# Kernel optimization log

Measured on AMD Instinct MI355X. Metric: run time of the kernel, lower is better.

Reference implementation:

```python
import jax, jax.numpy as jnp
import numpy as np

N_HEADS = 2
WINDOW = 4
BLOCK = 256


def _get_rel_emb(emb, length):
    # emb: [1, 2*WINDOW+1, K] -> [1, 2*length-1, K]
    pad = max(length - (WINDOW + 1), 0)
    start = max((WINDOW + 1) - length, 0)
    e = jnp.pad(emb, ((0, 0), (pad, pad), (0, 0)))
    return e[:, start:start + 2 * length - 1]


def _rel_to_abs(x):
    # x: [b, h, l, 2l-1] -> [b, h, l, l] (skew trick)
    b, h, l, _ = x.shape
    x = jnp.pad(x, ((0, 0), (0, 0), (0, 0), (0, 1))).reshape(b, h, 2 * l * l)
    x = jnp.pad(x, ((0, 0), (0, 0), (0, l - 1))).reshape(b, h, l + 1, 2 * l - 1)
    return x[:, :, :l, l - 1:]


def _abs_to_rel(x):
    # x: [b, h, l, l] -> [b, h, l, 2l-1] (inverse skew)
    b, h, l, _ = x.shape
    x = jnp.pad(x, ((0, 0), (0, 0), (0, 0), (0, l - 1))).reshape(b, h, l * (2 * l - 1))
    x = jnp.pad(x, ((0, 0), (0, 0), (l, 0))).reshape(b, h, l, 2 * l)
    return x[:, :, :, 1:]


def _attention(x, c, attn_mask, Wq, bq, Wk, bk, Wv, bv, Wo, bo, emb_rel_k, emb_rel_v):
    B, C, T = x.shape
    H, K = N_HEADS, C // N_HEADS
    # projections (torch Linear on [B,T,C])
    q = (jnp.einsum('bct,cd->btd', x, Wq) + bq).reshape(B, T, H, K).transpose(0, 2, 1, 3)
    k = (jnp.einsum('bct,cd->btd', c, Wk) + bk).reshape(B, T, H, K).transpose(0, 2, 1, 3)
    v = (jnp.einsum('bct,cd->btd', c, Wv) + bv).reshape(B, T, H, K).transpose(0, 2, 1, 3)
    qs = q / jnp.sqrt(jnp.float32(K))
    scores = jnp.einsum('bhtk,bhsk->bhts', qs, k)  # [B,H,T,T]
    # relative-position key logits (heads_share=True -> single table)
    rel_k = _get_rel_emb(emb_rel_k, T)[0]          # [2T-1, K]
    rel_logits = jnp.einsum('bhtk,rk->bhtr', qs, rel_k)
    scores = scores + _rel_to_abs(rel_logits)
    # proximal bias: -log1p(|i-j|)
    r = jnp.arange(T, dtype=jnp.float32)
    scores = scores - jnp.log1p(jnp.abs(r[:, None] - r[None, :]))[None, None]
    # attn mask + block-local mask (block mask active because mask is given)
    ij = jnp.arange(T)
    block_ok = jnp.abs(ij[:, None] - ij[None, :]) <= BLOCK
    valid = (attn_mask != 0) & block_ok[None, None]
    scores = jnp.where(valid, scores, jnp.float32(-1e4))
    p = jax.nn.softmax(scores, axis=-1)
    out = jnp.einsum('bhts,bhsk->bhtk', p, v)
    # relative-position value contribution
    rel_v = _get_rel_emb(emb_rel_v, T)[0]          # [2T-1, K]
    out = out + jnp.einsum('bhtr,rk->bhtk', _abs_to_rel(p), rel_v)
    out = out.transpose(0, 2, 1, 3).reshape(B, T, C)
    y = jnp.einsum('btd,do->bto', out, Wo) + bo
    return y.transpose(0, 2, 1)  # [B, out_channels, T]


def setup_inputs() -> dict:
    key = jax.random.key(0)
    ks = jax.random.split(key, 8)
    B, C, T = 4, 192, 2048
    K = C // N_HEADS
    s = jnp.float32(0.05)
    rel_std = jnp.float32(K ** -0.5)
    return {
        'x': jax.random.normal(ks[0], (B, C, T), jnp.float32),
        'c': jax.random.normal(ks[1], (B, C, T), jnp.float32),
        'Wq': jax.random.normal(ks[2], (C, C), jnp.float32) * s,
        'bq': jnp.zeros((C,), jnp.float32),
        'Wk': jax.random.normal(ks[3], (C, C), jnp.float32) * s,
        'bk': jnp.zeros((C,), jnp.float32),
        'Wv': jax.random.normal(ks[4], (C, C), jnp.float32) * s,
        'bv': jnp.zeros((C,), jnp.float32),
        'Wo': jax.random.normal(ks[5], (C, C), jnp.float32) * s,
        'bo': jnp.zeros((C,), jnp.float32),
        'emb_rel_k': jax.random.normal(ks[6], (1, 2 * WINDOW + 1, K), jnp.float32) * rel_std,
        'emb_rel_v': jax.random.normal(ks[7], (1, 2 * WINDOW + 1, K), jnp.float32) * rel_std,
        'attn_mask': jnp.ones((B, 1, T, T), jnp.int32),
    }


def reference(x, c, Wq, bq, Wk, bk, Wv, bv, Wo, bo, emb_rel_k, emb_rel_v, attn_mask):
    return _attention(x, c, attn_mask, Wq, bq, Wk, bk, Wv, bv, Wo, bo, emb_rel_k, emb_rel_v)
```

## Files before the change

### kernel.cpp

```cpp
#include <hip/hip_runtime.h>
#include <hip/hip_bf16.h>

#define B_DIM 4
#define C_DIM 192
#define T_SEQ 2048
#define H_DIM 2
#define K_DIM 96
#define BAND 256
#define IT 16
#define WSLOT 544
#define W_P 548
#define PMW 17

typedef __attribute__((ext_vector_type(8))) short bf16x8;
typedef __attribute__((ext_vector_type(4))) short bf16x4;
typedef __attribute__((ext_vector_type(4))) float f32x4;
#define MFMA16 __builtin_amdgcn_mfma_f32_16x16x32_bf16

__device__ __forceinline__ float bfbits2f(short s) {
    union { short s; __hip_bfloat16 h; } u; u.s = s; return __bfloat162float(u.h);
}
__device__ __forceinline__ short f2bf_bits(float f) {
    union { __hip_bfloat16 h; short s; } u; u.h = __float2bfloat16(f); return u.s;
}

#define OFF_WT(m)  ((size_t)(m)*73728)
#define OFF_BQS    ((size_t)294912)
#define OFF_RELKBF ((size_t)295680)
#define OFF_PM     ((size_t)298752)
#define OFF_QBF    ((size_t)855808)
#define OFF_KBF    (OFF_QBF + 3145728)
#define OFF_VTB    (OFF_KBF + 3145728)
#define OFF_OBTC   (OFF_VTB + 3145728)

__global__ __launch_bounds__(256)
void prep_kernel(const float* __restrict__ Wq, const float* __restrict__ Wk,
                 const float* __restrict__ Wv, const float* __restrict__ Wo,
                 const float* __restrict__ bq, const float* __restrict__ relk,
                 const int* __restrict__ mask, char* __restrict__ ws)
{
    const float qscale = 0.10206207261596577f;
    const int bidx = blockIdx.x;
    const int tid  = threadIdx.x;

    if (bidx < 576) {
        const size_t idx = (size_t)bidx*256 + tid;
        const int mi  = (int)(idx / 36864);
        const int rem = (int)(idx % 36864);
        const int c = rem / C_DIM, d = rem % C_DIM;
        const float* src = (mi == 0) ? Wq : (mi == 1) ? Wk : (mi == 2) ? Wv : Wo;
        float v = src[c*C_DIM + d];
        if (mi == 0) v *= qscale;
        ((short*)(ws + OFF_WT(mi)))[d*C_DIM + c] = f2bf_bits(v);
        return;
    }
    if (bidx < 1120) {
        const int idx = (bidx - 576)*256 + tid;
        const int b = idx / (T_SEQ*PMW);
        const int rem = idx % (T_SEQ*PMW);
        const int i = rem / PMW, w = rem % PMW;
        const int jlo = max(0, (i & ~15) - BAND);
        const int* mrow = mask + ((size_t)b*T_SEQ + i)*T_SEQ;
        unsigned bits = 0;
        #pragma unroll
        for (int g4 = 0; g4 < 8; ++g4) {
            const int jg = jlo + 32*w + 4*g4;
            if (jg + 3 < T_SEQ) {
                const int4 mv = *reinterpret_cast<const int4*>(mrow + jg);
                bits |= (unsigned)(mv.x != 0) << (4*g4);
                bits |= (unsigned)(mv.y != 0) << (4*g4+1);
                bits |= (unsigned)(mv.z != 0) << (4*g4+2);
                bits |= (unsigned)(mv.w != 0) << (4*g4+3);
            } else {
                #pragma unroll
                for (int e = 0; e < 4; ++e)
                    if (jg + e < T_SEQ && mrow[jg+e] != 0) bits |= 1u << (4*g4+e);
            }
        }
        ((unsigned*)(ws + OFF_PM))[idx] = bits;
        return;
    }
    if (tid < C_DIM)
        ((float*)(ws + OFF_BQS))[tid] = bq[tid]*qscale;
    short* rkb = (short*)(ws + OFF_RELKBF);
    for (int idx = tid; idx < 16*K_DIM; idx += 256) {
        const int row = idx / K_DIM;
        rkb[idx] = (row < 9) ? f2bf_bits(relk[idx]) : (short)0;
    }
}

__global__ __launch_bounds__(256)
void proj_kernel(const float* __restrict__ x, const float* __restrict__ cin,
                 const float* __restrict__ bk, const float* __restrict__ bv,
                 char* __restrict__ ws)
{
    __shared__ short xs[IT*C_DIM];
    __shared__ short cs[IT*C_DIM];
    const int b   = blockIdx.x >> 7;
    const int t0  = (blockIdx.x & 127) * IT;
    const int tid = threadIdx.x;
    const int wave = tid >> 6, lane = tid & 63;
    const int q4 = lane >> 4, lr = lane & 15;

    for (int l = tid; l < 768; l += 256) {
        const int cr = l >> 2, u = l & 3;
        const size_t off = (size_t)(b*C_DIM + cr)*T_SEQ + t0 + 4*u;
        const float4 xv = *reinterpret_cast<const float4*>(x + off);
        const float4 cv = *reinterpret_cast<const float4*>(cin + off);
        xs[(4*u+0)*C_DIM + cr] = f2bf_bits(xv.x);
        xs[(4*u+1)*C_DIM + cr] = f2bf_bits(xv.y);
        xs[(4*u+2)*C_DIM + cr] = f2bf_bits(xv.z);
        xs[(4*u+3)*C_DIM + cr] = f2bf_bits(xv.w);
        cs[(4*u+0)*C_DIM + cr] = f2bf_bits(cv.x);
        cs[(4*u+1)*C_DIM + cr] = f2bf_bits(cv.y);
        cs[(4*u+2)*C_DIM + cr] = f2bf_bits(cv.z);
        cs[(4*u+3)*C_DIM + cr] = f2bf_bits(cv.w);
    }
    __syncthreads();

    const short* WqT = (const short*)(ws + OFF_WT(0));
    const short* WkT = (const short*)(ws + OFF_WT(1));
    const short* WvT = (const short*)(ws + OFF_WT(2));

    f32x4 qa[3], ka[3], va[3];
    #pragma unroll
    for (int j = 0; j < 3; ++j) {
        qa[j] = (f32x4){0,0,0,0}; ka[j] = (f32x4){0,0,0,0}; va[j] = (f32x4){0,0,0,0};
    }
    for (int kc = 0; kc < 6; ++kc) {
        const int ko = kc*32 + q4*8;
        const bf16x8 xf = *reinterpret_cast<const bf16x8*>(xs + lr*C_DIM + ko);
        const bf16x8 cf = *reinterpret_cast<const bf16x8*>(cs + lr*C_DIM + ko);
        #pragma unroll
        for (int j = 0; j < 3; ++j) {
            const int dt = 3*wave + j;
            const bf16x8 wqf = *reinterpret_cast<const bf16x8*>(WqT + (dt*16 + lr)*C_DIM + ko);
            const bf16x8 wkf = *reinterpret_cast<const bf16x8*>(WkT + (dt*16 + lr)*C_DIM + ko);
            const bf16x8 wvf = *reinterpret_cast<const bf16x8*>(WvT + (dt*16 + lr)*C_DIM + ko);
            qa[j] = MFMA16(xf, wqf, qa[j], 0, 0, 0);
            ka[j] = MFMA16(cf, wkf, ka[j], 0, 0, 0);
            va[j] = MFMA16(wvf, cf, va[j], 0, 0, 0);
        }
    }

    const float* bqs = (const float*)(ws + OFF_BQS);
    short* qbf = (short*)(ws + OFF_QBF);
    short* kbf = (short*)(ws + OFF_KBF);
    short* vtb = (short*)(ws + OFF_VTB);
    #pragma unroll
    for (int j = 0; j < 3; ++j) {
        const int dt = 3*wave + j;
        {
            const int d = dt*16 + lr, h = d/K_DIM, kk = d%K_DIM;
            const int bh = b*H_DIM + h;
            const float bq_v = bqs[d], bk_v = bk[d];
            #pragma unroll
            for (int e = 0; e < 4; ++e) {
                const int t = t0 + q4*4 + e;
                const size_t off = ((size_t)bh*T_SEQ + t)*K_DIM + kk;
                qbf[off] = f2bf_bits(qa[j][e] + bq_v);
                kbf[off] = f2bf_bits(ka[j][e] + bk_v);
            }
        }
        {
            #pragma unroll
            for (int e = 0; e < 4; ++e) {
                const int d = dt*16 + q4*4 + e, h = d/K_DIM, kk = d%K_DIM;
                const int bh = b*H_DIM + h;
                vtb[((size_t)bh*K_DIM + kk)*T_SEQ + t0 + lr] = f2bf_bits(va[j][e] + bv[d]);
            }
        }
    }
}

__global__ __launch_bounds__(256)
void attn_kernel(const float* __restrict__ relv, char* __restrict__ ws)
{
    __shared__ float p_s[IT*W_P];
    __shared__ float shbuf[864];

    const short* qbf = (const short*)(ws + OFF_QBF);
    const short* kbf = (const short*)(ws + OFF_KBF);
    const short* vtb = (const short*)(ws + OFF_VTB);
    const short* rkb = (const short*)(ws + OFF_RELKBF);
    const unsigned* pm = (const unsigned*)(ws + OFF_PM);
    short* obtc = (short*)(ws + OFF_OBTC);

    const int bh  = blockIdx.x >> 7;
    const int i0  = (blockIdx.x & 127) * IT;
    const int b   = bh / H_DIM;
    const int h   = bh % H_DIM;
    const int tid = threadIdx.x;
    const int wave = tid >> 6, lane = tid & 63;
    const int q4 = lane >> 4, lr = lane & 15;

    const int jlo  = max(0, i0 - BAND);
    const int jhi  = min(T_SEQ - 1, i0 + IT - 1 + BAND);
    const int wlen = jhi - jlo + 1;
    const size_t qkv_base = (size_t)bh * T_SEQ * K_DIM;

    float* lt = shbuf;
    float* rl = shbuf + 260;
    for (int idx = tid; idx < 257; idx += 256) lt[idx] = log1pf((float)idx);

    bf16x8 qa[3];
    {
        const short* qrow = qbf + qkv_base + (size_t)(i0 + lr)*K_DIM + q4*8;
        #pragma unroll
        for (int kc = 0; kc < 3; ++kc)
            qa[kc] = *reinterpret_cast<const bf16x8*>(qrow + kc*32);
    }

    for (int jt = wave; jt < WSLOT/16; jt += 4) {
        int jr = jlo + jt*16 + lr;
        if (jr > T_SEQ-1) jr = T_SEQ-1;
        const short* krow = kbf + qkv_base + (size_t)jr*K_DIM + q4*8;
        f32x4 s = {0.f,0.f,0.f,0.f};
        #pragma unroll
        for (int kc = 0; kc < 3; ++kc)
            s = MFMA16(qa[kc], *reinterpret_cast<const bf16x8*>(krow + kc*32), s, 0, 0, 0);
        #pragma unroll
        for (int e = 0; e < 4; ++e)
            p_s[(q4*4 + e)*W_P + jt*16 + lr] = s[e];
    }
    if (wave == 3) {
        const short* krow = rkb + lr*K_DIM + q4*8;
        f32x4 s = {0.f,0.f,0.f,0.f};
        #pragma unroll
        for (int kc = 0; kc < 3; ++kc)
            s = MFMA16(qa[kc], *reinterpret_cast<const bf16x8*>(krow + kc*32), s, 0, 0, 0);
        if (lr < 9) {
            #pragma unroll
            for (int e = 0; e < 4; ++e)
                rl[(q4*4 + e)*9 + lr] = s[e];
        }
    }
    __syncthreads();

    {
        const int r = tid >> 4, sj = tid & 15;
        const int i = i0 + r;
        const int pmrow = (b*T_SEQ + i)*PMW;
        float vals[36];
        float m = -INFINITY;
        #pragma unroll
        for (int mm = 0; mm < 9; ++mm) {
            const int j0 = 4*sj + 64*mm;
            float4 pv = make_float4(0.f,0.f,0.f,0.f);
            unsigned mb = 0;
            if (j0 < WSLOT) {
                pv = *reinterpret_cast<const float4*>(p_s + r*W_P + j0);
                mb = pm[pmrow + (j0 >> 5)] >> (j0 & 31);
            }
            const float pe[4] = {pv.x, pv.y, pv.z, pv.w};
            #pragma unroll
            for (int e = 0; e < 4; ++e) {
                const int j = j0 + e;
                float val = -INFINITY;
                if (j0 < WSLOT && j < wlen) {
                    const int jg = jlo + j, dd = jg - i;
                    const int ad = dd < 0 ? -dd : dd;
                    if (ad <= BAND && ((mb >> e) & 1)) {
                        val = pe[e] - lt[ad];
                        if ((unsigned)(dd + 4) <= 8u) val += rl[r*9 + dd + 4];
                    }
                }
                vals[mm*4 + e] = val;
                m = fmaxf(m, val);
            }
        }
        #pragma unroll
        for (int off = 8; off > 0; off >>= 1) m = fmaxf(m, __shfl_xor(m, off, 64));
        if (m == -INFINITY) m = 0.f;
        float ssum = 0.f;
        #pragma unroll
        for (int u = 0; u < 36; ++u) { vals[u] = __expf(vals[u] - m); ssum += vals[u]; }
        #pragma unroll
        for (int off = 8; off > 0; off >>= 1) ssum += __shfl_xor(ssum, off, 64);
        const float inv = ssum > 0.f ? 1.f/ssum : 0.f;
        short* pb = (short*)p_s;
        #pragma unroll
        for (int mm = 0; mm < 9; ++mm) {
            const int j0 = 4*sj + 64*mm;
            if (j0 < WSLOT) {
                bf16x4 w;
                #pragma unroll
                for (int e = 0; e < 4; ++e) w[e] = f2bf_bits(vals[mm*4+e]*inv);
                *reinterpret_cast<bf16x4*>(pb + r*(2*W_P) + j0) = w;
            }
        }
    }
    __syncthreads();

    for (int idx = tid; idx < 9*K_DIM; idx += 256) shbuf[idx] = relv[idx];

    const short* pb = (const short*)p_s;
    f32x4 o0 = {0.f,0.f,0.f,0.f}, o1 = {0.f,0.f,0.f,0.f};
    for (int kc = 0; kc < WSLOT/32; ++kc) {
        const bf16x8 pa = *reinterpret_cast<const bf16x8*>(pb + lr*(2*W_P) + kc*32 + q4*8);
        int tc = jlo + kc*32 + q4*8;
        if (tc > T_SEQ-8) tc = T_SEQ-8;
        const bf16x8 vb0 = *reinterpret_cast<const bf16x8*>(
            vtb + qkv_base + (size_t)(wave*16 + lr)*T_SEQ + tc);
        o0 = MFMA16(pa, vb0, o0, 0, 0, 0);
        if (wave < 2) {
            const bf16x8 vb1 = *reinterpret_cast<const bf16x8*>(
                vtb + qkv_base + (size_t)((wave+4)*16 + lr)*T_SEQ + tc);
            o1 = MFMA16(pa, vb1, o1, 0, 0, 0);
        }
    }
    __syncthreads();

    #pragma unroll
    for (int u = 0; u < 2; ++u) {
        if (u == 1 && wave >= 2) break;
        const int nt = (u == 0) ? wave : wave + 4;
        const f32x4 oc = (u == 0) ? o0 : o1;
        const int col = nt*16 + lr;
        #pragma unroll
        for (int e = 0; e < 4; ++e) {
            const int row = q4*4 + e;
            const int i = i0 + row;
            float v = oc[e];
            #pragma unroll
            for (int dd = 0; dd < 9; ++dd) {
                const int jg = i + dd - 4;
                if (jg >= 0 && jg < T_SEQ)
                    v += bfbits2f(pb[row*(2*W_P) + (jg - jlo)]) * shbuf[dd*K_DIM + col];
            }
            obtc[((size_t)b*T_SEQ + i)*C_DIM + h*K_DIM + col] = f2bf_bits(v);
        }
    }
}

__global__ __launch_bounds__(256)
void oproj_kernel(const float* __restrict__ bo, float* __restrict__ y,
                  const char* __restrict__ ws)
{
    const int b   = blockIdx.x >> 7;
    const int t0  = (blockIdx.x & 127) * 16;
    const int tid = threadIdx.x;
    const int wave = tid >> 6, lane = tid & 63;
    const int q4 = lane >> 4, lr = lane & 15;

    const short* WoT  = (const short*)(ws + OFF_WT(3));
    const short* obtc = (const short*)(ws + OFF_OBTC);

    f32x4 a[3];
    #pragma unroll
    for (int j = 0; j < 3; ++j) a[j] = (f32x4){0.f,0.f,0.f,0.f};
    for (int kc = 0; kc < 6; ++kc) {
        const int ko = kc*32 + q4*8;
        const bf16x8 bf = *reinterpret_cast<const bf16x8*>(
            obtc + ((size_t)b*T_SEQ + t0 + lr)*C_DIM + ko);
        #pragma unroll
        for (int j = 0; j < 3; ++j) {
            const bf16x8 af = *reinterpret_cast<const bf16x8*>(
                WoT + ((3*wave + j)*16 + lr)*C_DIM + ko);
            a[j] = MFMA16(af, bf, a[j], 0, 0, 0);
        }
    }
    #pragma unroll
    for (int j = 0; j < 3; ++j) {
        #pragma unroll
        for (int e = 0; e < 4; ++e) {
            const int d = (3*wave + j)*16 + q4*4 + e;
            y[((size_t)b*C_DIM + d)*T_SEQ + t0 + lr] = a[j][e] + bo[d];
        }
    }
}

extern "C" void kernel_launch(void* const* d_in, const int* in_sizes, int n_in,
                              void* d_out, int out_size, void* d_ws, size_t ws_size,
                              hipStream_t stream)
{
    const float* x    = (const float*)d_in[0];
    const float* c    = (const float*)d_in[1];
    const float* Wq   = (const float*)d_in[2];
    const float* bq   = (const float*)d_in[3];
    const float* Wk   = (const float*)d_in[4];
    const float* bk   = (const float*)d_in[5];
    const float* Wv   = (const float*)d_in[6];
    const float* bv   = (const float*)d_in[7];
    const float* Wo   = (const float*)d_in[8];
    const float* bo   = (const float*)d_in[9];
    const float* relk = (const float*)d_in[10];
    const float* relv = (const float*)d_in[11];
    const int*   mask = (const int*)d_in[12];
    float*       y    = (float*)d_out;
    char*        ws   = (char*)d_ws;

    hipLaunchKernelGGL(prep_kernel, dim3(1121), dim3(256), 0, stream,
                       Wq, Wk, Wv, Wo, bq, relk, mask, ws);
    hipLaunchKernelGGL(proj_kernel, dim3(B_DIM*(T_SEQ/16)), dim3(256), 0, stream,
                       x, c, bk, bv, ws);
    hipLaunchKernelGGL(attn_kernel, dim3(B_DIM*H_DIM*(T_SEQ/IT)), dim3(256), 0, stream,
                       relv, ws);
    hipLaunchKernelGGL(oproj_kernel, dim3(B_DIM*(T_SEQ/16)), dim3(256), 0, stream,
                       bo, y, ws);
}
```

Before: 179.8 us.

## Fuse output projection into attention kernel looping over heads per block

The attention kernel now handles both heads for a 16-row tile in sequence, keeps the per-head outputs in shared memory, and applies the output projection directly, so the separate oproj kernel and its bf16 intermediate buffer in global memory go away. The mask bits and log1p table are staged into shared memory once per block, and the log1p table is precomputed in prep. Weight transposition in prep is vectorised to float4 loads. In exchange the attention grid is halved to 512 blocks, which lowers parallelism and raises shared memory use per block.

```diff
diff --git a/kernel.cpp b/kernel.cpp
--- a/kernel.cpp
+++ b/kernel.cpp
@@ -27,11 +27,14 @@
 #define OFF_WT(m)  ((size_t)(m)*73728)
 #define OFF_BQS    ((size_t)294912)
 #define OFF_RELKBF ((size_t)295680)
-#define OFF_PM     ((size_t)298752)
-#define OFF_QBF    ((size_t)855808)
+#define OFF_LT     ((size_t)298752)
+#define OFF_PM     ((size_t)299840)
+#define OFF_QBF    ((size_t)856896)
 #define OFF_KBF    (OFF_QBF + 3145728)
 #define OFF_VTB    (OFF_KBF + 3145728)
-#define OFF_OBTC   (OFF_VTB + 3145728)
+
+#define SH_RL   260
+#define SH_RELV 408
 
 __global__ __launch_bounds__(256)
 void prep_kernel(const float* __restrict__ Wq, const float* __restrict__ Wk,
@@ -43,19 +46,23 @@
     const int bidx = blockIdx.x;
     const int tid  = threadIdx.x;
 
-    if (bidx < 576) {
-        const size_t idx = (size_t)bidx*256 + tid;
-        const int mi  = (int)(idx / 36864);
-        const int rem = (int)(idx % 36864);
+    if (bidx < 144) {
+        const size_t idx4 = ((size_t)bidx*256 + tid)*4;
+        const int mi  = (int)(idx4 / 36864);
+        const int rem = (int)(idx4 % 36864);
         const int c = rem / C_DIM, d = rem % C_DIM;
         const float* src = (mi == 0) ? Wq : (mi == 1) ? Wk : (mi == 2) ? Wv : Wo;
-        float v = src[c*C_DIM + d];
-        if (mi == 0) v *= qscale;
-        ((short*)(ws + OFF_WT(mi)))[d*C_DIM + c] = f2bf_bits(v);
+        float4 v = *reinterpret_cast<const float4*>(src + c*C_DIM + d);
+        if (mi == 0) { v.x *= qscale; v.y *= qscale; v.z *= qscale; v.w *= qscale; }
+        short* wt = (short*)(ws + OFF_WT(mi));
+        wt[(d+0)*C_DIM + c] = f2bf_bits(v.x);
+        wt[(d+1)*C_DIM + c] = f2bf_bits(v.y);
+        wt[(d+2)*C_DIM + c] = f2bf_bits(v.z);
+        wt[(d+3)*C_DIM + c] = f2bf_bits(v.w);
         return;
     }
-    if (bidx < 1120) {
-        const int idx = (bidx - 576)*256 + tid;
+    if (bidx < 688) {
+        const int idx = (bidx - 144)*256 + tid;
         const int b = idx / (T_SEQ*PMW);
         const int rem = idx % (T_SEQ*PMW);
         const int i = rem / PMW, w = rem % PMW;
@@ -87,6 +94,8 @@
         const int row = idx / K_DIM;
         rkb[idx] = (row < 9) ? f2bf_bits(relk[idx]) : (short)0;
     }
+    float* ltws = (float*)(ws + OFF_LT);
+    for (int idx = tid; idx < 257; idx += 256) ltws[idx] = log1pf((float)idx);
 }
 
 __global__ __launch_bounds__(256)
@@ -174,22 +183,23 @@
 }
 
 __global__ __launch_bounds__(256)
-void attn_kernel(const float* __restrict__ relv, char* __restrict__ ws)
+void attn_kernel(const float* __restrict__ relv, const float* __restrict__ bo,
+                 float* __restrict__ y, char* __restrict__ ws)
 {
     __shared__ float p_s[IT*W_P];
-    __shared__ float shbuf[864];
+    __shared__ float shbuf[1272];
+    __shared__ unsigned pml[IT*PMW];
+    __shared__ __align__(16) short ob[IT*C_DIM];
 
     const short* qbf = (const short*)(ws + OFF_QBF);
     const short* kbf = (const short*)(ws + OFF_KBF);
     const short* vtb = (const short*)(ws + OFF_VTB);
     const short* rkb = (const short*)(ws + OFF_RELKBF);
+    const float* ltws = (const float*)(ws + OFF_LT);
     const unsigned* pm = (const unsigned*)(ws + OFF_PM);
-    short* obtc = (short*)(ws + OFF_OBTC);
-
-    const int bh  = blockIdx.x >> 7;
+
+    const int b   = blockIdx.x >> 7;
     const int i0  = (blockIdx.x & 127) * IT;
-    const int b   = bh / H_DIM;
-    const int h   = bh % H_DIM;
     const int tid = threadIdx.x;
     const int wave = tid >> 6, lane = tid & 63;
     const int q4 = lane >> 4, lr = lane & 15;
@@ -197,175 +207,161 @@
     const int jlo  = max(0, i0 - BAND);
     const int jhi  = min(T_SEQ - 1, i0 + IT - 1 + BAND);
     const int wlen = jhi - jlo + 1;
-    const size_t qkv_base = (size_t)bh * T_SEQ * K_DIM;
 
     float* lt = shbuf;
-    float* rl = shbuf + 260;
-    for (int idx = tid; idx < 257; idx += 256) lt[idx] = log1pf((float)idx);
-
-    bf16x8 qa[3];
-    {
-        const short* qrow = qbf + qkv_base + (size_t)(i0 + lr)*K_DIM + q4*8;
-        #pragma unroll
-        for (int kc = 0; kc < 3; ++kc)
-            qa[kc] = *reinterpret_cast<const bf16x8*>(qrow + kc*32);
-    }
-
-    for (int jt = wave; jt < WSLOT/16; jt += 4) {
-        int jr = jlo + jt*16 + lr;
-        if (jr > T_SEQ-1) jr = T_SEQ-1;
-        const short* krow = kbf + qkv_base + (size_t)jr*K_DIM + q4*8;
-        f32x4 s = {0.f,0.f,0.f,0.f};
-        #pragma unroll
-        for (int kc = 0; kc < 3; ++kc)
-            s = MFMA16(qa[kc], *reinterpret_cast<const bf16x8*>(krow + kc*32), s, 0, 0, 0);
-        #pragma unroll
-        for (int e = 0; e < 4; ++e)
-            p_s[(q4*4 + e)*W_P + jt*16 + lr] = s[e];
-    }
-    if (wave == 3) {
-        const short* krow = rkb + lr*K_DIM + q4*8;
-        f32x4 s = {0.f,0.f,0.f,0.f};
-        #pragma unroll
-        for (int kc = 0; kc < 3; ++kc)
-            s = MFMA16(qa[kc], *reinterpret_cast<const bf16x8*>(krow + kc*32), s, 0, 0, 0);
-        if (lr < 9) {
+    float* rl = shbuf + SH_RL;
+    float* rv = shbuf + SH_RELV;
+    for (int idx = tid; idx < 257; idx += 256) lt[idx] = ltws[idx];
+    for (int idx = tid; idx < IT*PMW; idx += 256)
+        pml[idx] = pm[(b*T_SEQ + i0)*PMW + idx];
+    for (int idx = tid; idx < 9*K_DIM; idx += 256) rv[idx] = relv[idx];
+
+    for (int h = 0; h < H_DIM; ++h) {
+        const size_t qkv_base = (size_t)(b*H_DIM + h) * T_SEQ * K_DIM;
+
+        bf16x8 qa[3];
+        {
+            const short* qrow = qbf + qkv_base + (size_t)(i0 + lr)*K_DIM + q4*8;
+            #pragma unroll
+            for (int kc = 0; kc < 3; ++kc)
+                qa[kc] = *reinterpret_cast<const bf16x8*>(qrow + kc*32);
+        }
+
+        for (int jt = wave; jt < WSLOT/16; jt += 4) {
+            int jr = jlo + jt*16 + lr;
+            if (jr > T_SEQ-1) jr = T_SEQ-1;
+            const short* krow = kbf + qkv_base + (size_t)jr*K_DIM + q4*8;
+            f32x4 s = {0.f,0.f,0.f,0.f};
+            #pragma unroll
+            for (int kc = 0; kc < 3; ++kc)
+                s = MFMA16(qa[kc], *reinterpret_cast<const bf16x8*>(krow + kc*32), s, 0, 0, 0);
             #pragma unroll
             for (int e = 0; e < 4; ++e)
-                rl[(q4*4 + e)*9 + lr] = s[e];
-        }
-    }
-    __syncthreads();
-
-    {
-        const int r = tid >> 4, sj = tid & 15;
-        const int i = i0 + r;
-        const int pmrow = (b*T_SEQ + i)*PMW;
-        float vals[36];
-        float m = -INFINITY;
-        #pragma unroll
-        for (int mm = 0; mm < 9; ++mm) {
-            const int j0 = 4*sj + 64*mm;
-            float4 pv = make_float4(0.f,0.f,0.f,0.f);
-            unsigned mb = 0;
-            if (j0 < WSLOT) {
-                pv = *reinterpret_cast<const float4*>(p_s + r*W_P + j0);
-                mb = pm[pmrow + (j0 >> 5)] >> (j0 & 31);
-            }
-            const float pe[4] = {pv.x, pv.y, pv.z, pv.w};
+                p_s[(q4*4 + e)*W_P + jt*16 + lr] = s[e];
+        }
+        if (wave == 3) {
+            const short* krow = rkb + lr*K_DIM + q4*8;
+            f32x4 s = {0.f,0.f,0.f,0.f};
+            #pragma unroll
+            for (int kc = 0; kc < 3; ++kc)
+                s = MFMA16(qa[kc], *reinterpret_cast<const bf16x8*>(krow + kc*32), s, 0, 0, 0);
+            if (lr < 9) {
+                #pragma unroll
+                for (int e = 0; e < 4; ++e)
+                    rl[(q4*4 + e)*9 + lr] = s[e];
+            }
+        }
+        __syncthreads();
+
+        {
+            const int r = tid >> 4, sj = tid & 15;
+            const int i = i0 + r;
+            float vals[36];
+            float m = -INFINITY;
+            #pragma unroll
+            for (int mm = 0; mm < 9; ++mm) {
+                const int j0 = 4*sj + 64*mm;
+                float4 pv = make_float4(0.f,0.f,0.f,0.f);
+                unsigned mb = 0;
+                if (j0 < WSLOT) {
+                    pv = *reinterpret_cast<const float4*>(p_s + r*W_P + j0);
+                    mb = pml[r*PMW + (j0 >> 5)] >> (j0 & 31);
+                }
+                const float pe[4] = {pv.x, pv.y, pv.z, pv.w};
+                #pragma unroll
+                for (int e = 0; e < 4; ++e) {
+                    const int j = j0 + e;
+                    float val = -INFINITY;
+                    if (j0 < WSLOT && j < wlen) {
+                        const int jg = jlo + j, dd = jg - i;
+                        const int ad = dd < 0 ? -dd : dd;
+                        if (ad <= BAND && ((mb >> e) & 1)) {
+                            val = pe[e] - lt[ad];
+                            if ((unsigned)(dd + 4) <= 8u) val += rl[r*9 + dd + 4];
+                        }
+                    }
+                    vals[mm*4 + e] = val;
+                    m = fmaxf(m, val);
+                }
+            }
+            #pragma unroll
+            for (int off = 8; off > 0; off >>= 1) m = fmaxf(m, __shfl_xor(m, off, 64));
+            if (m == -INFINITY) m = 0.f;
+            float ssum = 0.f;
+            #pragma unroll
+            for (int u = 0; u < 36; ++u) { vals[u] = __expf(vals[u] - m); ssum += vals[u]; }
+            #pragma unroll
+            for (int off = 8; off > 0; off >>= 1) ssum += __shfl_xor(ssum, off, 64);
+            const float inv = ssum > 0.f ? 1.f/ssum : 0.f;
+            short* pb = (short*)p_s;
+            #pragma unroll
+            for (int mm = 0; mm < 9; ++mm) {
+                const int j0 = 4*sj + 64*mm;
+                if (j0 < WSLOT) {
+                    bf16x4 w;
+                    #pragma unroll
+                    for (int e = 0; e < 4; ++e) w[e] = f2bf_bits(vals[mm*4+e]*inv);
+                    *reinterpret_cast<bf16x4*>(pb + r*(2*W_P) + j0) = w;
+                }
+            }
+        }
+        __syncthreads();
+
+        const short* pb = (const short*)p_s;
+        f32x4 o0 = {0.f,0.f,0.f,0.f}, o1 = {0.f,0.f,0.f,0.f};
+        for (int kc = 0; kc < WSLOT/32; ++kc) {
+            const bf16x8 pa = *reinterpret_cast<const bf16x8*>(pb + lr*(2*W_P) + kc*32 + q4*8);
+            int tc = jlo + kc*32 + q4*8;
+            if (tc > T_SEQ-8) tc = T_SEQ-8;
+            const bf16x8 vb0 = *reinterpret_cast<const bf16x8*>(
+                vtb + qkv_base + (size_t)(wave*16 + lr)*T_SEQ + tc);
+            o0 = MFMA16(pa, vb0, o0, 0, 0, 0);
+            if (wave < 2) {
+                const bf16x8 vb1 = *reinterpret_cast<const bf16x8*>(
+                    vtb + qkv_base + (size_t)((wave+4)*16 + lr)*T_SEQ + tc);
+                o1 = MFMA16(pa, vb1, o1, 0, 0, 0);
+            }
+        }
+
+        #pragma unroll
+        for (int u = 0; u < 2; ++u) {
+            if (u == 1 && wave >= 2) break;
+            const int nt = (u == 0) ? wave : wave + 4;
+            const f32x4 oc = (u == 0) ? o0 : o1;
+            const int col = nt*16 + lr;
             #pragma unroll
             for (int e = 0; e < 4; ++e) {
-                const int j = j0 + e;
-                float val = -INFINITY;
-                if (j0 < WSLOT && j < wlen) {
-                    const int jg = jlo + j, dd = jg - i;
-                    const int ad = dd < 0 ? -dd : dd;
-                    if (ad <= BAND && ((mb >> e) & 1)) {
-                        val = pe[e] - lt[ad];
-                        if ((unsigned)(dd + 4) <= 8u) val += rl[r*9 + dd + 4];
-                    }
+                const int row = q4*4 + e;
+                const int i = i0 + row;
+                float v = oc[e];
+                #pragma unroll
+                for (int dd = 0; dd < 9; ++dd) {
+                    const int jg = i + dd - 4;
+                    if (jg >= 0 && jg < T_SEQ)
+                        v += bfbits2f(pb[row*(2*W_P) + (jg - jlo)]) * rv[dd*K_DIM + col];
                 }
-                vals[mm*4 + e] = val;
-                m = fmaxf(m, val);
-            }
-        }
-        #pragma unroll
-        for (int off = 8; off > 0; off >>= 1) m = fmaxf(m, __shfl_xor(m, off, 64));
-        if (m == -INFINITY) m = 0.f;
-        float ssum = 0.f;
-        #pragma unroll
-        for (int u = 0; u < 36; ++u) { vals[u] = __expf(vals[u] - m); ssum += vals[u]; }
-        #pragma unroll
-        for (int off = 8; off > 0; off >>= 1) ssum += __shfl_xor(ssum, off, 64);
-        const float inv = ssum > 0.f ? 1.f/ssum : 0.f;
-        short* pb = (short*)p_s;
-        #pragma unroll
-        for (int mm = 0; mm < 9; ++mm) {
-            const int j0 = 4*sj + 64*mm;
-            if (j0 < WSLOT) {
-                bf16x4 w;
-                #pragma unroll
-                for (int e = 0; e < 4; ++e) w[e] = f2bf_bits(vals[mm*4+e]*inv);
-                *reinterpret_cast<bf16x4*>(pb + r*(2*W_P) + j0) = w;
-            }
-        }
-    }
-    __syncthreads();
-
-    for (int idx = tid; idx < 9*K_DIM; idx += 256) shbuf[idx] = relv[idx];
-
-    const short* pb = (const short*)p_s;
-    f32x4 o0 = {0.f,0.f,0.f,0.f}, o1 = {0.f,0.f,0.f,0.f};
-    for (int kc = 0; kc < WSLOT/32; ++kc) {
-        const bf16x8 pa = *reinterpret_cast<const bf16x8*>(pb + lr*(2*W_P) + kc*32 + q4*8);
-        int tc = jlo + kc*32 + q4*8;
-        if (tc > T_SEQ-8) tc = T_SEQ-8;
-        const bf16x8 vb0 = *reinterpret_cast<const bf16x8*>(
-            vtb + qkv_base + (size_t)(wave*16 + lr)*T_SEQ + tc);
-        o0 = MFMA16(pa, vb0, o0, 0, 0, 0);
-        if (wave < 2) {
-            const bf16x8 vb1 = *reinterpret_cast<const bf16x8*>(
-                vtb + qkv_base + (size_t)((wave+4)*16 + lr)*T_SEQ + tc);
-            o1 = MFMA16(pa, vb1, o1, 0, 0, 0);
-        }
-    }
-    __syncthreads();
-
-    #pragma unroll
-    for (int u = 0; u < 2; ++u) {
-        if (u == 1 && wave >= 2) break;
-        const int nt = (u == 0) ? wave : wave + 4;
-        const f32x4 oc = (u == 0) ? o0 : o1;
-        const int col = nt*16 + lr;
-        #pragma unroll
-        for (int e = 0; e < 4; ++e) {
-            const int row = q4*4 + e;
-            const int i = i0 + row;
-            float v = oc[e];
-            #pragma unroll
-            for (int dd = 0; dd < 9; ++dd) {
-                const int jg = i + dd - 4;
-                if (jg >= 0 && jg < T_SEQ)
-                    v += bfbits2f(pb[row*(2*W_P) + (jg - jlo)]) * shbuf[dd*K_DIM + col];
-            }
-            obtc[((size_t)b*T_SEQ + i)*C_DIM + h*K_DIM + col] = f2bf_bits(v);
-        }
-    }
-}
-
-__global__ __launch_bounds__(256)
-void oproj_kernel(const float* __restrict__ bo, float* __restrict__ y,
-                  const char* __restrict__ ws)
-{
-    const int b   = blockIdx.x >> 7;
-    const int t0  = (blockIdx.x & 127) * 16;
-    const int tid = threadIdx.x;
-    const int wave = tid >> 6, lane = tid & 63;
-    const int q4 = lane >> 4, lr = lane & 15;
-
-    const short* WoT  = (const short*)(ws + OFF_WT(3));
-    const short* obtc = (const short*)(ws + OFF_OBTC);
-
-    f32x4 a[3];
-    #pragma unroll
-    for (int j = 0; j < 3; ++j) a[j] = (f32x4){0.f,0.f,0.f,0.f};
-    for (int kc = 0; kc < 6; ++kc) {
-        const int ko = kc*32 + q4*8;
-        const bf16x8 bf = *reinterpret_cast<const bf16x8*>(
-            obtc + ((size_t)b*T_SEQ + t0 + lr)*C_DIM + ko);
-        #pragma unroll
-        for (int j = 0; j < 3; ++j) {
-            const bf16x8 af = *reinterpret_cast<const bf16x8*>(
-                WoT + ((3*wave + j)*16 + lr)*C_DIM + ko);
-            a[j] = MFMA16(af, bf, a[j], 0, 0, 0);
-        }
-    }
+                ob[row*C_DIM + h*K_DIM + col] = f2bf_bits(v);
+            }
+        }
+        __syncthreads();
+    }
+
+    const short* WoT = (const short*)(ws + OFF_WT(3));
     #pragma unroll
     for (int j = 0; j < 3; ++j) {
+        const int dt = 3*wave + j;
+        f32x4 a = {0.f,0.f,0.f,0.f};
+        #pragma unroll
+        for (int kc = 0; kc < 6; ++kc) {
+            const int ko = kc*32 + q4*8;
+            const bf16x8 bf = *reinterpret_cast<const bf16x8*>(ob + lr*C_DIM + ko);
+            const bf16x8 af = *reinterpret_cast<const bf16x8*>(WoT + (dt*16 + lr)*C_DIM + ko);
+            a = MFMA16(af, bf, a, 0, 0, 0);
+        }
         #pragma unroll
         for (int e = 0; e < 4; ++e) {
-            const int d = (3*wave + j)*16 + q4*4 + e;
-            y[((size_t)b*C_DIM + d)*T_SEQ + t0 + lr] = a[j][e] + bo[d];
+            const int d = dt*16 + q4*4 + e;
+            y[((size_t)b*C_DIM + d)*T_SEQ + i0 + lr] = a[e] + bo[d];
         }
     }
 }
@@ -390,12 +386,10 @@
     float*       y    = (float*)d_out;
     char*        ws   = (char*)d_ws;
 
-    hipLaunchKernelGGL(prep_kernel, dim3(1121), dim3(256), 0, stream,
+    hipLaunchKernelGGL(prep_kernel, dim3(689), dim3(256), 0, stream,
                        Wq, Wk, Wv, Wo, bq, relk, mask, ws);
     hipLaunchKernelGGL(proj_kernel, dim3(B_DIM*(T_SEQ/16)), dim3(256), 0, stream,
                        x, c, bk, bv, ws);
-    hipLaunchKernelGGL(attn_kernel, dim3(B_DIM*H_DIM*(T_SEQ/IT)), dim3(256), 0, stream,
-                       relv, ws);
-    hipLaunchKernelGGL(oproj_kernel, dim3(B_DIM*(T_SEQ/16)), dim3(256), 0, stream,
-                       bo, y, ws);
-}
+    hipLaunchKernelGGL(attn_kernel, dim3(B_DIM*(T_SEQ/IT)), dim3(256), 0, stream,
+                       relv, bo, y, ws);
+}
```

Result: slower. 186.6 us (+3.8%).
